# Performance work log

Measured on AMD Instinct MI355X. Metric: run time of the kernel, lower is better.

Reference implementation:

```python
import jax, jax.numpy as jnp
import numpy as np

N_NODES = 50000


def gcn_conv(x, W, b, src, dst):
    # PyG GCNConv: lin (no bias) -> add self-loops -> symmetric deg norm ->
    # scatter-add messages to target nodes -> add bias.
    n = x.shape[0]
    xw = x @ W  # [N, H]
    loops = jnp.arange(n, dtype=src.dtype)
    s = jnp.concatenate([src, loops])
    d = jnp.concatenate([dst, loops])
    deg = jax.ops.segment_sum(jnp.ones(d.shape[0], dtype=x.dtype), d, num_segments=n)
    dinv = deg ** -0.5  # deg >= 1 due to self-loops
    norm = dinv[s] * dinv[d]  # [E+N]
    msg = xw[s] * norm[:, None]  # gather + scale, [E+N, H]
    out = jax.ops.segment_sum(msg, d, num_segments=n)  # scatter-add
    return out + b


def setup_inputs() -> dict:
    key = jax.random.key(0)
    ks = jax.random.split(key, 8)
    in_feats, hidden, out_feats, p = 64, 64, 32, 4
    x = jax.random.normal(ks[0], (N_NODES, in_feats), dtype=jnp.float32)
    edge_index = jax.random.randint(ks[1], (2, 800000), 0, N_NODES, dtype=jnp.int64)
    s1 = (1.0 / in_feats) ** 0.5
    s2 = (1.0 / hidden) ** 0.5
    W1 = jax.random.uniform(ks[2], (in_feats, hidden), jnp.float32, -s1, s1)
    b1 = jnp.zeros((hidden,), jnp.float32)
    W2 = jax.random.uniform(ks[3], (hidden, hidden), jnp.float32, -s2, s2)
    b2 = jnp.zeros((hidden,), jnp.float32)
    Wr = jax.random.uniform(ks[4], (hidden, out_feats * p), jnp.float32, -s2, s2)
    br = jax.random.uniform(ks[5], (out_feats * p,), jnp.float32, -s2, s2)
    return {"x": x, "edge_index": edge_index, "W1": W1, "b1": b1,
            "W2": W2, "b2": b2, "Wr": Wr, "br": br}


def reference(x, edge_index, W1, b1, W2, b2, Wr, br):
    src, dst = edge_index[0], edge_index[1]
    h = jax.nn.relu(gcn_conv(x, W1, b1, src, dst))
    h = jax.nn.relu(gcn_conv(h, W2, b2, src, dst))
    g = jnp.mean(h, axis=0, keepdims=True)  # [1, hidden]
    out = (g @ Wr + br).reshape(32, 4)  # (out_feats, p)
    return out
```

## Files before the change

kernel.cpp:

```cpp
#include <hip/hip_runtime.h>
#include <math.h>


#define CH 4096
#define MAXNB 1024

__device__ __forceinline__ float bf2f(unsigned short u) {
    return __uint_as_float(((unsigned)u) << 16);
}
__device__ __forceinline__ unsigned short f2bf(float x) {
    unsigned b = __float_as_uint(x);
    return (unsigned short)((b + 0x7FFF + ((b >> 16) & 1)) >> 16);
}

__global__ __launch_bounds__(256) void k_bucket_hist(const int* __restrict__ dst,
                                                     int* __restrict__ histmat,
                                                     int E, int NB) {
    __shared__ int ih[MAXNB];
    int t = threadIdx.x;
    for (int k = t; k < NB; k += 256) ih[k] = 0;
    __syncthreads();
    int base = blockIdx.x * CH;
    for (int i = 0; i < CH; i += 256) {
        int e = base + i + t;
        if (e < E) atomicAdd(&ih[dst[e] >> 6], 1);
    }
    __syncthreads();
    for (int k = t; k < NB; k += 256) histmat[(size_t)blockIdx.x * NB + k] = ih[k];
}

__global__ __launch_bounds__(256) void k_colscan(int* __restrict__ histmat,
                                                 int* __restrict__ tot,
                                                 int NB, int nch) {
    int k = blockIdx.x * 256 + threadIdx.x;
    if (k >= NB) return;
    int run = 0;
    int b = 0;
    for (; b + 8 <= nch; b += 8) {
        int v[8];
#pragma unroll
        for (int u = 0; u < 8; u++) v[u] = histmat[(size_t)(b + u) * NB + k];
#pragma unroll
        for (int u = 0; u < 8; u++) {
            int x = v[u];
            histmat[(size_t)(b + u) * NB + k] = run;
            run += x;
        }
    }
    for (; b < nch; b++) {
        int x = histmat[(size_t)b * NB + k];
        histmat[(size_t)b * NB + k] = run;
        run += x;
    }
    tot[k] = run;
}

__global__ __launch_bounds__(256) void k_scanb(const int* __restrict__ tot,
                                               int* __restrict__ bstart,
                                               int* __restrict__ offsets,
                                               int NB, int E, int n) {
    __shared__ int sc[256];
    __shared__ int carry;
    int t = threadIdx.x;
    if (t == 0) carry = 0;
    __syncthreads();
    int nchunk = (NB + 255) / 256;
    for (int c = 0; c < nchunk; c++) {
        int idx = c * 256 + t;
        int v = (idx < NB) ? tot[idx] : 0;
        sc[t] = v;
        __syncthreads();
        for (int off = 1; off < 256; off <<= 1) {
            int x = (t >= off) ? sc[t - off] : 0;
            __syncthreads();
            sc[t] += x;
            __syncthreads();
        }
        if (idx < NB) bstart[idx] = sc[t] - v + carry;
        __syncthreads();
        if (t == 0) carry += sc[255];
        __syncthreads();
    }
    if (t == 0) { bstart[NB] = E; offsets[n] = E; }
}

__global__ __launch_bounds__(256) void k_bucket_scatter(const int* __restrict__ src,
                                                        const int* __restrict__ dst,
                                                        const int* __restrict__ histmat,
                                                        const int* __restrict__ bstart,
                                                        int* __restrict__ staged,
                                                        int E, int NB) {
    __shared__ int cur[MAXNB];
    int t = threadIdx.x;
    for (int k = t; k < NB; k += 256)
        cur[k] = bstart[k] + histmat[(size_t)blockIdx.x * NB + k];
    __syncthreads();
    int base = blockIdx.x * CH;
    for (int i = 0; i < CH; i += 256) {
        int e = base + i + t;
        if (e < E) {
            int d = dst[e];
            int pos = atomicAdd(&cur[d >> 6], 1);
            staged[pos] = (src[e] << 6) | (d & 63);
        }
    }
}

__global__ __launch_bounds__(256) void k_local_sort(const int* __restrict__ staged,
                                                    const int* __restrict__ bstart,
                                                    unsigned short* __restrict__ csr,
                                                    int* __restrict__ offsets,
                                                    float* __restrict__ dinv, int n) {
    __shared__ int cnt[64];
    __shared__ int pos[64];
    __shared__ int cur[64];
    int t = threadIdx.x;
    if (t < 64) cnt[t] = 0;
    __syncthreads();
    int k = blockIdx.x;
    int beg = bstart[k], end = bstart[k + 1];
    for (int e = beg + t; e < end; e += 256) atomicAdd(&cnt[staged[e] & 63], 1);
    __syncthreads();
    if (t == 0) {
        int run = 0;
        for (int i = 0; i < 64; i++) { pos[i] = run; run += cnt[i]; }
    }
    __syncthreads();
    if (t < 64) {
        cur[t] = pos[t];
        int node = k * 64 + t;
        if (node < n) {
            offsets[node] = beg + pos[t];
            dinv[node] = 1.0f / sqrtf((float)(cnt[t] + 1));
        }
    }
    __syncthreads();
    for (int e = beg + t; e < end; e += 256) {
        int pk = staged[e];
        int p = atomicAdd(&cur[pk & 63], 1);
        csr[beg + p] = (unsigned short)(pk >> 6);
    }
}

template <bool BIN>
__global__ __launch_bounds__(256) void k_gemm_scale(const void* __restrict__ Xv,
                                                    const float* __restrict__ W,
                                                    const float* __restrict__ dinv,
                                                    unsigned short* __restrict__ Y, int n) {
    __shared__ float Ws[64 * 64];
    __shared__ float xs[16][64];
    int t = threadIdx.x, w = t >> 6, f = t & 63;
    const float4* W4 = (const float4*)W;
    float4* Ws4 = (float4*)Ws;
#pragma unroll
    for (int j = 0; j < 4; j++) Ws4[t + 256 * j] = W4[t + 256 * j];
    int r0 = blockIdx.x * 16;
#pragma unroll
    for (int i = 0; i < 4; i++) {
        int r = r0 + w * 4 + i;
        float v = 0.f;
        if (r < n)
            v = BIN ? bf2f(((const unsigned short*)Xv)[(size_t)r * 64 + f])
                    : ((const float*)Xv)[(size_t)r * 64 + f];
        xs[w * 4 + i][f] = v;
    }
    __syncthreads();
    float acc[4] = {0.f, 0.f, 0.f, 0.f};
#pragma unroll 8
    for (int k = 0; k < 64; k++) {
        float wv = Ws[k * 64 + f];
#pragma unroll
        for (int i = 0; i < 4; i++) acc[i] += xs[w * 4 + i][k] * wv;
    }
#pragma unroll
    for (int i = 0; i < 4; i++) {
        int r = r0 + w * 4 + i;
        if (r < n) Y[(size_t)r * 64 + f] = f2bf(dinv[r] * acc[i]);
    }
}

template <bool POOL>
__global__ __launch_bounds__(256) void k_aggregate(const unsigned short* __restrict__ Y,
                                                   const float* __restrict__ dinv,
                                                   const float* __restrict__ bias,
                                                   const int* __restrict__ offsets,
                                                   const unsigned short* __restrict__ csr,
                                                   unsigned short* __restrict__ H,
                                                   float* __restrict__ pbuf, int n) {
    __shared__ float4 sm4[4][16];
    const ushort4* Y4 = (const ushort4*)Y;
    int t = threadIdx.x, w = t >> 6, l = t & 63;
    int q = l >> 4, c = l & 15;
    int node = blockIdx.x * 4 + w;
    bool valid = node < n;
    float4 hval = make_float4(0.f, 0.f, 0.f, 0.f);
    if (valid) {
        float4 acc = make_float4(0.f, 0.f, 0.f, 0.f);
        if (q == 0) {
            ushort4 u = Y4[(size_t)node * 16 + c];
            acc = make_float4(bf2f(u.x), bf2f(u.y), bf2f(u.z), bf2f(u.w));
        }
        int beg = offsets[node], end = offsets[node + 1];
        for (int j = beg + q; j < end; j += 16) {
#pragma unroll
            for (int u = 0; u < 4; u++) {
                int jj = j + 4 * u;
                if (jj < end) {
                    int s = csr[jj];
                    ushort4 v = Y4[(size_t)s * 16 + c];
                    acc.x += bf2f(v.x); acc.y += bf2f(v.y);
                    acc.z += bf2f(v.z); acc.w += bf2f(v.w);
                }
            }
        }
#pragma unroll
        for (int m = 16; m <= 32; m <<= 1) {
            acc.x += __shfl_xor(acc.x, m);
            acc.y += __shfl_xor(acc.y, m);
            acc.z += __shfl_xor(acc.z, m);
            acc.w += __shfl_xor(acc.w, m);
        }
        float dv = dinv[node];
        float4 b4 = ((const float4*)bias)[c];
        hval.x = fmaxf(dv * acc.x + b4.x, 0.f);
        hval.y = fmaxf(dv * acc.y + b4.y, 0.f);
        hval.z = fmaxf(dv * acc.z + b4.z, 0.f);
        hval.w = fmaxf(dv * acc.w + b4.w, 0.f);
        if (!POOL && q == 0) {
            ushort4 o;
            o.x = f2bf(hval.x); o.y = f2bf(hval.y);
            o.z = f2bf(hval.z); o.w = f2bf(hval.w);
            ((ushort4*)H)[(size_t)node * 16 + c] = o;
        }
    }
    if (POOL) {
        if (q == 0) sm4[w][c] = valid ? hval : make_float4(0.f, 0.f, 0.f, 0.f);
        __syncthreads();
        if (t < 16) {
            float4 a = sm4[0][t], b = sm4[1][t], d = sm4[2][t], e = sm4[3][t];
            float4 s;
            s.x = (a.x + b.x) + (d.x + e.x);
            s.y = (a.y + b.y) + (d.y + e.y);
            s.z = (a.z + b.z) + (d.z + e.z);
            s.w = (a.w + b.w) + (d.w + e.w);
            ((float4*)pbuf)[(size_t)blockIdx.x * 16 + t] = s;
        }
    }
}

__global__ void k_mean_final(const float* __restrict__ pbuf, float* __restrict__ g,
                             int nrows) {
    __shared__ float part[256];
    int t = threadIdx.x, w = t >> 6, f = t & 63;
    float local = 0.f;
    for (int r = blockIdx.x * 4 + w; r < nrows; r += gridDim.x * 4)
        local += pbuf[(size_t)r * 64 + f];
    part[t] = local;
    __syncthreads();
    if (w == 0) {
        float tot = part[f] + part[64 + f] + part[128 + f] + part[192 + f];
        atomicAdd(&g[f], tot);
    }
}

__global__ void k_readout(const float* __restrict__ g, const float* __restrict__ Wr,
                          const float* __restrict__ br, float* __restrict__ out,
                          float invn) {
    __shared__ float gl[64];
    int t = threadIdx.x;
    if (t < 64) gl[t] = g[t] * invn;
    __syncthreads();
    float acc = br[t];
#pragma unroll
    for (int k = 0; k < 64; k++) acc += gl[k] * Wr[k * 128 + t];
    out[t] = acc;
}

extern "C" void kernel_launch(void* const* d_in, const int* in_sizes, int n_in,
                              void* d_out, int out_size, void* d_ws, size_t ws_size,
                              hipStream_t stream) {
    const float* x  = (const float*)d_in[0];
    const int*   ei = (const int*)d_in[1];
    const float* W1 = (const float*)d_in[2];
    const float* b1 = (const float*)d_in[3];
    const float* W2 = (const float*)d_in[4];
    const float* b2 = (const float*)d_in[5];
    const float* Wr = (const float*)d_in[6];
    const float* br = (const float*)d_in[7];
    float* out = (float*)d_out;

    int n = in_sizes[0] / 64;
    int E = in_sizes[1] / 2;
    const int* src = ei;
    const int* dst = ei + E;

    int NB  = (n + 63) / 64;
    int nch = (E + CH - 1) / CH;

    char* p = (char*)d_ws;
    unsigned short* y1 = (unsigned short*)p; p += (size_t)n * 64 * sizeof(unsigned short);
    unsigned short* y2 = (unsigned short*)p; p += (size_t)n * 64 * sizeof(unsigned short);
    float* pbuf = (float*)p;   p += (size_t)((n + 3) / 4) * 64 * sizeof(float);
    float* dinv = (float*)p;   p += (size_t)n * sizeof(float);
    float* g = (float*)p;      p += 64 * sizeof(float);
    int* staged = (int*)p;     p += (size_t)E * sizeof(int);
    int* offsets = (int*)p;    p += (size_t)(n + 1) * sizeof(int);
    int* histmat = (int*)p;    p += (size_t)nch * NB * sizeof(int);
    int* tot = (int*)p;        p += (size_t)NB * sizeof(int);
    int* bstart = (int*)p;     p += (size_t)(NB + 1) * sizeof(int);
    unsigned short* csr = (unsigned short*)p; p += (size_t)E * sizeof(unsigned short);

    hipMemsetAsync(g, 0, 64 * sizeof(float), stream);
    k_bucket_hist<<<nch, 256, 0, stream>>>(dst, histmat, E, NB);
    k_colscan<<<(NB + 255) / 256, 256, 0, stream>>>(histmat, tot, NB, nch);
    k_scanb<<<1, 256, 0, stream>>>(tot, bstart, offsets, NB, E, n);
    k_bucket_scatter<<<nch, 256, 0, stream>>>(src, dst, histmat, bstart, staged, E, NB);
    k_local_sort<<<NB, 256, 0, stream>>>(staged, bstart, csr, offsets, dinv, n);

    int gb = (n + 3) / 4;
    k_gemm_scale<false><<<(n + 15) / 16, 256, 0, stream>>>(x, W1, dinv, y1, n);
    k_aggregate<false><<<gb, 256, 0, stream>>>(y1, dinv, b1, offsets, csr, y2, nullptr, n);
    k_gemm_scale<true><<<(n + 15) / 16, 256, 0, stream>>>(y2, W2, dinv, y1, n);
    k_aggregate<true><<<gb, 256, 0, stream>>>(y1, dinv, b2, offsets, csr, nullptr, pbuf, n);

    k_mean_final<<<64, 256, 0, stream>>>(pbuf, g, gb);
    k_readout<<<1, 128, 0, stream>>>(g, Wr, br, out, 1.0f / (float)n);
}
```

Before: 231.1 us.

## Fuse layer-2 GEMM into layer-1 aggregation and merge scan kernels

Layer-1 aggregation now applies ReLU and multiplies by W2 (scaled by dinv) in the same kernel. This removes the separate GEMM launch and the bf16 round trip of the hidden activations through memory. The column scan and bucket-offset scan are merged into one 1024-thread single-block kernel, which also zeroes the pooled accumulator, replacing a memset and a launch. The costs are that each aggregation block now loads the full 16KB W2 into shared memory, and the single-block scan serialises all column scans onto one workgroup.

```diff
diff --git a/kernel.cpp b/kernel.cpp
--- a/kernel.cpp
+++ b/kernel.cpp
@@ -29,59 +29,44 @@
     for (int k = t; k < NB; k += 256) histmat[(size_t)blockIdx.x * NB + k] = ih[k];
 }
 
-__global__ __launch_bounds__(256) void k_colscan(int* __restrict__ histmat,
-                                                 int* __restrict__ tot,
-                                                 int NB, int nch) {
-    int k = blockIdx.x * 256 + threadIdx.x;
-    if (k >= NB) return;
-    int run = 0;
-    int b = 0;
-    for (; b + 8 <= nch; b += 8) {
-        int v[8];
-#pragma unroll
-        for (int u = 0; u < 8; u++) v[u] = histmat[(size_t)(b + u) * NB + k];
-#pragma unroll
-        for (int u = 0; u < 8; u++) {
-            int x = v[u];
-            histmat[(size_t)(b + u) * NB + k] = run;
-            run += x;
-        }
-    }
-    for (; b < nch; b++) {
-        int x = histmat[(size_t)b * NB + k];
-        histmat[(size_t)b * NB + k] = run;
-        run += x;
-    }
-    tot[k] = run;
-}
-
-__global__ __launch_bounds__(256) void k_scanb(const int* __restrict__ tot,
+__global__ __launch_bounds__(1024) void k_scan(int* __restrict__ histmat,
                                                int* __restrict__ bstart,
                                                int* __restrict__ offsets,
-                                               int NB, int E, int n) {
-    __shared__ int sc[256];
-    __shared__ int carry;
-    int t = threadIdx.x;
-    if (t == 0) carry = 0;
-    __syncthreads();
-    int nchunk = (NB + 255) / 256;
-    for (int c = 0; c < nchunk; c++) {
-        int idx = c * 256 + t;
-        int v = (idx < NB) ? tot[idx] : 0;
-        sc[t] = v;
+                                               float* __restrict__ g,
+                                               int NB, int nch, int E, int n) {
+    __shared__ int sc[1024];
+    int t = threadIdx.x;
+    int run = 0;
+    if (t < NB) {
+        int b = 0;
+        for (; b + 8 <= nch; b += 8) {
+            int v[8];
+#pragma unroll
+            for (int u = 0; u < 8; u++) v[u] = histmat[(size_t)(b + u) * NB + t];
+#pragma unroll
+            for (int u = 0; u < 8; u++) {
+                int x = v[u];
+                histmat[(size_t)(b + u) * NB + t] = run;
+                run += x;
+            }
+        }
+        for (; b < nch; b++) {
+            int x = histmat[(size_t)b * NB + t];
+            histmat[(size_t)b * NB + t] = run;
+            run += x;
+        }
+    }
+    sc[t] = (t < NB) ? run : 0;
+    __syncthreads();
+    for (int off = 1; off < 1024; off <<= 1) {
+        int x = (t >= off) ? sc[t - off] : 0;
         __syncthreads();
-        for (int off = 1; off < 256; off <<= 1) {
-            int x = (t >= off) ? sc[t - off] : 0;
-            __syncthreads();
-            sc[t] += x;
-            __syncthreads();
-        }
-        if (idx < NB) bstart[idx] = sc[t] - v + carry;
+        sc[t] += x;
         __syncthreads();
-        if (t == 0) carry += sc[255];
-        __syncthreads();
-    }
+    }
+    if (t < NB) bstart[t] = sc[t] - run;
     if (t == 0) { bstart[NB] = E; offsets[n] = E; }
+    if (t < 64) g[t] = 0.f;
 }
 
 __global__ __launch_bounds__(256) void k_bucket_scatter(const int* __restrict__ src,
@@ -142,8 +127,7 @@
     }
 }
 
-template <bool BIN>
-__global__ __launch_bounds__(256) void k_gemm_scale(const void* __restrict__ Xv,
+__global__ __launch_bounds__(256) void k_gemm_scale(const float* __restrict__ X,
                                                     const float* __restrict__ W,
                                                     const float* __restrict__ dinv,
                                                     unsigned short* __restrict__ Y, int n) {
@@ -158,11 +142,7 @@
 #pragma unroll
     for (int i = 0; i < 4; i++) {
         int r = r0 + w * 4 + i;
-        float v = 0.f;
-        if (r < n)
-            v = BIN ? bf2f(((const unsigned short*)Xv)[(size_t)r * 64 + f])
-                    : ((const float*)Xv)[(size_t)r * 64 + f];
-        xs[w * 4 + i][f] = v;
+        xs[w * 4 + i][f] = (r < n) ? X[(size_t)r * 64 + f] : 0.f;
     }
     __syncthreads();
     float acc[4] = {0.f, 0.f, 0.f, 0.f};
@@ -179,14 +159,81 @@
     }
 }
 
-template <bool POOL>
-__global__ __launch_bounds__(256) void k_aggregate(const unsigned short* __restrict__ Y,
-                                                   const float* __restrict__ dinv,
-                                                   const float* __restrict__ bias,
-                                                   const int* __restrict__ offsets,
-                                                   const unsigned short* __restrict__ csr,
-                                                   unsigned short* __restrict__ H,
-                                                   float* __restrict__ pbuf, int n) {
+__global__ __launch_bounds__(256) void k_agg_fuse(const unsigned short* __restrict__ Y,
+                                                  const float* __restrict__ dinv,
+                                                  const float* __restrict__ bias,
+                                                  const int* __restrict__ offsets,
+                                                  const unsigned short* __restrict__ csr,
+                                                  const float* __restrict__ W2,
+                                                  unsigned short* __restrict__ Yout, int n) {
+    __shared__ float Ws[64 * 64];
+    __shared__ float hs[4][64];
+    const ushort4* Y4 = (const ushort4*)Y;
+    int t = threadIdx.x, w = t >> 6, l = t & 63;
+    int q = l >> 4, c = l & 15;
+    {
+        const float4* W4 = (const float4*)W2;
+        float4* Ws4 = (float4*)Ws;
+#pragma unroll
+        for (int j = 0; j < 4; j++) Ws4[t + 256 * j] = W4[t + 256 * j];
+    }
+    int node = blockIdx.x * 4 + w;
+    bool valid = node < n;
+    float4 hval = make_float4(0.f, 0.f, 0.f, 0.f);
+    float dv = 0.f;
+    if (valid) {
+        float4 acc = make_float4(0.f, 0.f, 0.f, 0.f);
+        if (q == 0) {
+            ushort4 u = Y4[(size_t)node * 16 + c];
+            acc = make_float4(bf2f(u.x), bf2f(u.y), bf2f(u.z), bf2f(u.w));
+        }
+        int beg = offsets[node], end = offsets[node + 1];
+        for (int j = beg + q; j < end; j += 16) {
+#pragma unroll
+            for (int u = 0; u < 4; u++) {
+                int jj = j + 4 * u;
+                if (jj < end) {
+                    int s = csr[jj];
+                    ushort4 v = Y4[(size_t)s * 16 + c];
+                    acc.x += bf2f(v.x); acc.y += bf2f(v.y);
+                    acc.z += bf2f(v.z); acc.w += bf2f(v.w);
+                }
+            }
+        }
+#pragma unroll
+        for (int m = 16; m <= 32; m <<= 1) {
+            acc.x += __shfl_xor(acc.x, m);
+            acc.y += __shfl_xor(acc.y, m);
+            acc.z += __shfl_xor(acc.z, m);
+            acc.w += __shfl_xor(acc.w, m);
+        }
+        dv = dinv[node];
+        float4 b4 = ((const float4*)bias)[c];
+        hval.x = fmaxf(dv * acc.x + b4.x, 0.f);
+        hval.y = fmaxf(dv * acc.y + b4.y, 0.f);
+        hval.z = fmaxf(dv * acc.z + b4.z, 0.f);
+        hval.w = fmaxf(dv * acc.w + b4.w, 0.f);
+    }
+    if (q == 0) ((float4*)hs[w])[c] = hval;
+    __syncthreads();
+    if (valid) {
+        float acc2 = 0.f;
+#pragma unroll
+        for (int m = 0; m < 16; m++) {
+            float4 h4 = ((const float4*)hs[w])[m];
+            acc2 += h4.x * Ws[(4 * m + 0) * 64 + l] + h4.y * Ws[(4 * m + 1) * 64 + l]
+                  + h4.z * Ws[(4 * m + 2) * 64 + l] + h4.w * Ws[(4 * m + 3) * 64 + l];
+        }
+        Yout[(size_t)node * 64 + l] = f2bf(dv * acc2);
+    }
+}
+
+__global__ __launch_bounds__(256) void k_agg_pool(const unsigned short* __restrict__ Y,
+                                                  const float* __restrict__ dinv,
+                                                  const float* __restrict__ bias,
+                                                  const int* __restrict__ offsets,
+                                                  const unsigned short* __restrict__ csr,
+                                                  float* __restrict__ pbuf, int n) {
     __shared__ float4 sm4[4][16];
     const ushort4* Y4 = (const ushort4*)Y;
     int t = threadIdx.x, w = t >> 6, l = t & 63;
@@ -226,25 +273,17 @@
         hval.y = fmaxf(dv * acc.y + b4.y, 0.f);
         hval.z = fmaxf(dv * acc.z + b4.z, 0.f);
         hval.w = fmaxf(dv * acc.w + b4.w, 0.f);
-        if (!POOL && q == 0) {
-            ushort4 o;
-            o.x = f2bf(hval.x); o.y = f2bf(hval.y);
-            o.z = f2bf(hval.z); o.w = f2bf(hval.w);
-            ((ushort4*)H)[(size_t)node * 16 + c] = o;
-        }
-    }
-    if (POOL) {
-        if (q == 0) sm4[w][c] = valid ? hval : make_float4(0.f, 0.f, 0.f, 0.f);
-        __syncthreads();
-        if (t < 16) {
-            float4 a = sm4[0][t], b = sm4[1][t], d = sm4[2][t], e = sm4[3][t];
-            float4 s;
-            s.x = (a.x + b.x) + (d.x + e.x);
-            s.y = (a.y + b.y) + (d.y + e.y);
-            s.z = (a.z + b.z) + (d.z + e.z);
-            s.w = (a.w + b.w) + (d.w + e.w);
-            ((float4*)pbuf)[(size_t)blockIdx.x * 16 + t] = s;
-        }
+    }
+    if (q == 0) sm4[w][c] = valid ? hval : make_float4(0.f, 0.f, 0.f, 0.f);
+    __syncthreads();
+    if (t < 16) {
+        float4 a = sm4[0][t], b = sm4[1][t], d = sm4[2][t], e = sm4[3][t];
+        float4 s;
+        s.x = (a.x + b.x) + (d.x + e.x);
+        s.y = (a.y + b.y) + (d.y + e.y);
+        s.z = (a.z + b.z) + (d.z + e.z);
+        s.w = (a.w + b.w) + (d.w + e.w);
+        ((float4*)pbuf)[(size_t)blockIdx.x * 16 + t] = s;
     }
 }
 
@@ -306,22 +345,18 @@
     int* staged = (int*)p;     p += (size_t)E * sizeof(int);
     int* offsets = (int*)p;    p += (size_t)(n + 1) * sizeof(int);
     int* histmat = (int*)p;    p += (size_t)nch * NB * sizeof(int);
-    int* tot = (int*)p;        p += (size_t)NB * sizeof(int);
     int* bstart = (int*)p;     p += (size_t)(NB + 1) * sizeof(int);
     unsigned short* csr = (unsigned short*)p; p += (size_t)E * sizeof(unsigned short);
 
-    hipMemsetAsync(g, 0, 64 * sizeof(float), stream);
     k_bucket_hist<<<nch, 256, 0, stream>>>(dst, histmat, E, NB);
-    k_colscan<<<(NB + 255) / 256, 256, 0, stream>>>(histmat, tot, NB, nch);
-    k_scanb<<<1, 256, 0, stream>>>(tot, bstart, offsets, NB, E, n);
+    k_scan<<<1, 1024, 0, stream>>>(histmat, bstart, offsets, g, NB, nch, E, n);
     k_bucket_scatter<<<nch, 256, 0, stream>>>(src, dst, histmat, bstart, staged, E, NB);
     k_local_sort<<<NB, 256, 0, stream>>>(staged, bstart, csr, offsets, dinv, n);
 
     int gb = (n + 3) / 4;
-    k_gemm_scale<false><<<(n + 15) / 16, 256, 0, stream>>>(x, W1, dinv, y1, n);
-    k_aggregate<false><<<gb, 256, 0, stream>>>(y1, dinv, b1, offsets, csr, y2, nullptr, n);
-    k_gemm_scale<true><<<(n + 15) / 16, 256, 0, stream>>>(y2, W2, dinv, y1, n);
-    k_aggregate<true><<<gb, 256, 0, stream>>>(y1, dinv, b2, offsets, csr, nullptr, pbuf, n);
+    k_gemm_scale<<<(n + 15) / 16, 256, 0, stream>>>(x, W1, dinv, y1, n);
+    k_agg_fuse<<<gb, 256, 0, stream>>>(y1, dinv, b1, offsets, csr, W2, y2, n);
+    k_agg_pool<<<gb, 256, 0, stream>>>(y2, dinv, b2, offsets, csr, pbuf, n);
 
     k_mean_final<<<64, 256, 0, stream>>>(pbuf, g, gb);
     k_readout<<<1, 128, 0, stream>>>(g, Wr, br, out, 1.0f / (float)n);
```

Measured after the change: 229.9 us. No clear change (-0.5%).
